# Kernel optimization log

Measured on AMD Instinct MI355X. Metric: run time of the kernel, lower is better.

## Reference

```python
import jax, jax.numpy as jnp
import numpy as np

NUM_HEADS = 16
ROPE_BASE = 10000.0


def _rope_tables(head_dim, seq_len, dtype=jnp.float32):
    # Half-split convention: rotate first half against second half.
    inv_freq = 1.0 / (ROPE_BASE ** (jnp.arange(0, head_dim, 2, dtype=dtype) / head_dim))
    pos = jnp.arange(seq_len, dtype=dtype)
    angles_half = jnp.einsum('s,d->sd', pos, inv_freq)          # (S, D/2)
    angles = jnp.concatenate([angles_half, angles_half], -1)     # (S, D)
    return jnp.cos(angles), jnp.sin(angles)


def _apply_rope(x, cos, sin):
    # x: (H, S, D); cos/sin: (S, D) broadcast over heads
    half = x.shape[-1] // 2
    x1, x2 = x[..., :half], x[..., half:]
    x_rot = jnp.concatenate([-x2, x1], axis=-1)
    return x * cos + x_rot * sin


def setup_inputs() -> dict:
    key = jax.random.key(0)
    S, E = 2048, 2048
    ks = jax.random.split(key, 9)
    sc = 0.02
    return {
        'x': jax.random.normal(ks[0], (S, E), jnp.float32),
        'Wq': jax.random.normal(ks[1], (E, E), jnp.float32) * sc,
        'bq': jax.random.normal(ks[2], (E,), jnp.float32) * sc,
        'Wk': jax.random.normal(ks[3], (E, E), jnp.float32) * sc,
        'bk': jax.random.normal(ks[4], (E,), jnp.float32) * sc,
        'Wv': jax.random.normal(ks[5], (E, E), jnp.float32) * sc,
        'bv': jax.random.normal(ks[6], (E,), jnp.float32) * sc,
        'Wo': jax.random.normal(ks[7], (E, E), jnp.float32) * sc,
        'bo': jax.random.normal(ks[8], (E,), jnp.float32) * sc,
    }


def reference(x, Wq, bq, Wk, bk, Wv, bv, Wo, bo):
    S, E = x.shape
    H = NUM_HEADS
    D = E // H
    scale = D ** 0.5
    cos, sin = _rope_tables(D, S, x.dtype)

    def proj(W, b):
        return (x @ W.T + b).reshape(S, H, D).transpose(1, 0, 2)  # (H, S, D)

    q = _apply_rope(proj(Wq, bq), cos, sin)
    k = _apply_rope(proj(Wk, bk), cos, sin)
    v = proj(Wv, bv)

    scores = jnp.einsum('hsd,htd->hst', q, k) / scale  # (H, S, S)
    attn = jax.nn.softmax(scores, axis=-1)
    out = jnp.einsum('hst,htd->hsd', attn, v)          # (H, S, D)
    # Faithful to the original's transpose(0,1).view(S,E) on a (1,H,S,D)
    # tensor: an in-order (head-major) flatten reinterpreted as (S, E).
    out = out.reshape(S, E)
    return out @ Wo.T + bo
```

## Files before the change

### kernel.cpp

```cpp
#include <hip/hip_runtime.h>

#define SDIM 2048
#define EDIM 2048
#define NHEAD 16
#define DHEAD 128

typedef __attribute__((ext_vector_type(8))) short short8;
typedef __attribute__((ext_vector_type(4))) float floatx4;

__device__ __forceinline__ float bf2f(ushort u) {
    union { uint i; float f; } v; v.i = ((uint)u) << 16; return v.f;
}
__device__ __forceinline__ ushort f2bf(float f) {
    union { float f; uint i; } v; v.f = f;
    uint r = v.i + 0x7fff + ((v.i >> 16) & 1);
    return (ushort)(r >> 16);
}

__device__ __forceinline__ void gload_lds16(const ushort* g, ushort* l) {
    __builtin_amdgcn_global_load_lds(
        (const __attribute__((address_space(1))) void*)g,
        (__attribute__((address_space(3))) void*)l, 16, 0, 0);
}

__global__ void convert5_kernel(
    const float* __restrict__ s0, const float* __restrict__ s1,
    const float* __restrict__ s2, const float* __restrict__ s3,
    const float* __restrict__ s4,
    ushort* __restrict__ d0, ushort* __restrict__ d1,
    ushort* __restrict__ d2, ushort* __restrict__ d3,
    ushort* __restrict__ d4)
{
    const float* src; ushort* dst;
    switch (blockIdx.y) {
        case 0: src = s0; dst = d0; break;
        case 1: src = s1; dst = d1; break;
        case 2: src = s2; dst = d2; break;
        case 3: src = s3; dst = d3; break;
        default: src = s4; dst = d4; break;
    }
    int i = blockIdx.x * blockDim.x + threadIdx.x;
    float4 f = ((const float4*)src)[i];
    ushort4 o;
    o.x = f2bf(f.x); o.y = f2bf(f.y); o.z = f2bf(f.z); o.w = f2bf(f.w);
    ((ushort4*)dst)[i] = o;
}

#define QPRESCALE 0.12754245f

__global__ __launch_bounds__(512, 2) void gemm256_qkv(
    const ushort* __restrict__ A,
    const ushort* __restrict__ B0, const ushort* __restrict__ B1, const ushort* __restrict__ B2,
    const float* __restrict__ s0, const float* __restrict__ s1, const float* __restrict__ s2,
    ushort* __restrict__ C0, ushort* __restrict__ C1, ushort* __restrict__ Vtg)
{
    __shared__ __align__(16) ushort smem[2][2][2][128 * 64];

    const int tid  = threadIdx.x;
    const int lane = tid & 63;
    const int wave = tid >> 6;
    const int l15 = lane & 15, quad = lane >> 4, l7 = lane & 7;
    const int wm = wave & 1, wn = wave >> 1;
    const int bm = blockIdx.x * 256;
    const int which = blockIdx.y >> 3;
    const int n0 = (blockIdx.y & 7) * 256;

    const ushort* Bsel = (which == 0) ? B0 : (which == 1) ? B1 : B2;
    const float*  bia  = (which == 0) ? s0 : (which == 1) ? s1 : s2;

    const int srow = tid >> 3;
    const int sgc  = (((tid & 7) ^ ((tid >> 3) & 7)) << 3);

    floatx4 acc[8][4];
#pragma unroll
    for (int i = 0; i < 8; i++)
#pragma unroll
        for (int j = 0; j < 4; j++) acc[i][j] = (floatx4)0.0f;

    auto stageA = [&](int tile, int h) {
        const ushort* g = A + (size_t)(bm + h * 128 + srow) * EDIM + tile * 64 + sgc;
        ushort* l = &smem[tile & 1][0][h][0] + tid * 8;
        gload_lds16(g, l);
        gload_lds16(g + (size_t)64 * EDIM, l + 4096);
    };
    auto stageB = [&](int tile, int h) {
        const ushort* g = Bsel + (size_t)(n0 + h * 128 + srow) * EDIM + tile * 64 + sgc;
        ushort* l = &smem[tile & 1][1][h][0] + tid * 8;
        gload_lds16(g, l);
        gload_lds16(g + (size_t)64 * EDIM, l + 4096);
    };

    stageA(0, 0); stageA(0, 1); stageB(0, 0); stageB(0, 1);
    stageB(1, 0); stageB(1, 1);
    asm volatile("s_waitcnt vmcnt(4)" ::: "memory");
    __builtin_amdgcn_s_barrier();

    const int c0 = ((quad ^ l7) << 3);
    const int c1 = (((quad + 4) ^ l7) << 3);
    const int brow0 = (wn & 1) * 64;

    short8 af[4][2], bq0[2][2], bq1[2][2];

#define MFMA8(AOFF, NOFF, BQ) \
    _Pragma("unroll") \
    for (int kk = 0; kk < 2; kk++) \
        _Pragma("unroll") \
        for (int mf = 0; mf < 4; mf++) \
            _Pragma("unroll") \
            for (int nf = 0; nf < 2; nf++) \
                acc[(AOFF) + mf][(NOFF) + nf] = __builtin_amdgcn_mfma_f32_16x16x32_bf16( \
                    af[mf][kk], BQ[nf][kk], acc[(AOFF) + mf][(NOFF) + nf], 0, 0, 0);

#define PH_PRE() do { \
    asm volatile("" ::: "memory"); \
    __builtin_amdgcn_s_barrier(); \
    asm volatile("s_waitcnt lgkmcnt(0)" ::: "memory"); \
    __builtin_amdgcn_sched_barrier(0); \
    __builtin_amdgcn_s_setprio(1); \
} while (0)
#define PH_POST() do { \
    __builtin_amdgcn_s_setprio(0); \
    asm volatile("" ::: "memory"); \
    __builtin_amdgcn_s_barrier(); \
} while (0)

    const int NTILES = EDIM / 64;
    for (int t = 0; t < NTILES; ++t) {
        const ushort* aH = &smem[t & 1][0][wm][0];
        const ushort* bH = &smem[t & 1][1][wn >> 1][0];

#pragma unroll
        for (int mf = 0; mf < 4; mf++) {
            const ushort* p = aH + (mf * 16 + l15) * 64;
            af[mf][0] = *(const short8*)(p + c0);
            af[mf][1] = *(const short8*)(p + c1);
        }
#pragma unroll
        for (int nf = 0; nf < 2; nf++) {
            const ushort* p = bH + (brow0 + nf * 16 + l15) * 64;
            bq0[nf][0] = *(const short8*)(p + c0);
            bq0[nf][1] = *(const short8*)(p + c1);
        }
        if (t + 1 < NTILES) stageA(t + 1, 0);
        PH_PRE();
        MFMA8(0, 0, bq0);
        PH_POST();

#pragma unroll
        for (int nf = 0; nf < 2; nf++) {
            const ushort* p = bH + (brow0 + 32 + nf * 16 + l15) * 64;
            bq1[nf][0] = *(const short8*)(p + c0);
            bq1[nf][1] = *(const short8*)(p + c1);
        }
        if (t + 1 < NTILES) stageA(t + 1, 1);
        PH_PRE();
        MFMA8(0, 2, bq1);
        PH_POST();

#pragma unroll
        for (int mf = 0; mf < 4; mf++) {
            const ushort* p = aH + (64 + mf * 16 + l15) * 64;
            af[mf][0] = *(const short8*)(p + c0);
            af[mf][1] = *(const short8*)(p + c1);
        }
        if (t + 2 < NTILES) stageB(t + 2, 0);
        PH_PRE();
        MFMA8(4, 2, bq1);
        PH_POST();

        if (t + 2 < NTILES) stageB(t + 2, 1);
        asm volatile("" ::: "memory");
        __builtin_amdgcn_s_barrier();
        __builtin_amdgcn_s_setprio(1);
        MFMA8(4, 0, bq0);
        __builtin_amdgcn_s_setprio(0);
        if (t < NTILES - 2) asm volatile("s_waitcnt vmcnt(4)" ::: "memory");
        else                asm volatile("s_waitcnt vmcnt(0)" ::: "memory");
        __builtin_amdgcn_s_barrier();
    }
#undef MFMA8
#undef PH_PRE
#undef PH_POST

    if (which == 2) {
#pragma unroll
        for (int an = 0; an < 4; an++) {
            int col = n0 + wn * 64 + an * 16 + l15;
            int h = col >> 7, d = col & 127;
            float bv = bia[col];
            ushort* cp = Vtg + (size_t)h * SDIM * DHEAD + (size_t)d * SDIM;
#pragma unroll
            for (int am = 0; am < 8; am++) {
                int s = bm + wm * 128 + am * 16 + quad * 4;
                ushort4 pk;
                pk.x = f2bf(acc[am][an][0] + bv);
                pk.y = f2bf(acc[am][an][1] + bv);
                pk.z = f2bf(acc[am][an][2] + bv);
                pk.w = f2bf(acc[am][an][3] + bv);
                *(ushort4*)(cp + s) = pk;
            }
        }
    } else {
        ushort* C = (which == 0) ? C0 : C1;
        const float psc = (which == 0) ? QPRESCALE : 1.0f;
        float* xch = (float*)smem;
        float bv[4], invf[4];
#pragma unroll
        for (int an = 0; an < 4; an++) {
            bv[an]   = bia[n0 + wn * 64 + an * 16 + l15];
            invf[an] = __expf((float)(an * 16 + l15) * -0.14391157f);
        }
        const int mybase = wave * 1024 + quad * 16 + l15;
        const int pbase  = (wave ^ 2) * 1024 + quad * 16 + l15;
        const int rowb = bm + wm * 128 + quad * 4;
#pragma unroll
        for (int am = 0; am < 8; am++) {
            __syncthreads();
#pragma unroll
            for (int an = 0; an < 4; an++)
#pragma unroll
                for (int r = 0; r < 4; r++)
                    xch[mybase + an * 256 + r * 64] = acc[am][an][r] + bv[an];
            __syncthreads();
#pragma unroll
            for (int an = 0; an < 4; an++) {
                int col = n0 + wn * 64 + an * 16 + l15;
#pragma unroll
                for (int r = 0; r < 4; r++) {
                    int row = rowb + am * 16 + r;
                    float v = acc[am][an][r] + bv[an];
                    float w = xch[pbase + an * 256 + r * 64];
                    float ang = (float)row * invf[an];
                    float rev = ang * 0.15915494309f;
                    rev -= floorf(rev);
                    float arad = rev * 6.28318530718f;
                    float sn = __sinf(arad), cs = __cosf(arad);
                    float o = ((wn & 1) == 0) ? (v * cs - w * sn) : (v * cs + w * sn);
                    C[(size_t)row * EDIM + col] = f2bf(o * psc);
                }
            }
        }
    }
}

template <typename OUTT, int KSPLIT, int VT_WHICH, bool ROPE>
__global__ __launch_bounds__(256) void gemm_bt(
    const ushort* __restrict__ A,
    const ushort* __restrict__ B0, const ushort* __restrict__ B1, const ushort* __restrict__ B2,
    const float* __restrict__ s0, const float* __restrict__ s1, const float* __restrict__ s2,
    OUTT* __restrict__ C0, OUTT* __restrict__ C1, OUTT* __restrict__ C2,
    int nbpm)
{
    __shared__ __align__(16) ushort smem[2 * 128 * 32];
    ushort* a_s = smem;
    ushort* b_s = smem + 128 * 32;

    const int tid = threadIdx.x;
    const int wave = tid >> 6, lane = tid & 63;
    const int l15 = lane & 15, quad = lane >> 4;
    const int wm = wave & 1, wn = wave >> 1;
    const int bm = blockIdx.x * 128;
    const int which = blockIdx.y / nbpm;
    const int n0 = (blockIdx.y % nbpm) * 128;

    const ushort* B;
    const float*  bia;
    OUTT*         C;
    const ushort* Abase;
    if constexpr (KSPLIT == 2) {
        B = B0; bia = s0; C = C0;
        Abase = A + which * (EDIM / 2);
    } else {
        B   = (which == 0) ? B0 : (which == 1) ? B1 : B2;
        bia = (which == 0) ? s0 : (which == 1) ? s1 : s2;
        C   = (which == 0) ? C0 : (which == 1) ? C1 : C2;
        Abase = A;
    }
    const ushort* Bbase = (KSPLIT == 2) ? B + which * (EDIM / 2) : B;

    floatx4 acc[4][4];
#pragma unroll
    for (int i = 0; i < 4; i++)
#pragma unroll
        for (int j = 0; j < 4; j++) acc[i][j] = (floatx4)0.0f;

    const int t1 = tid + 256;
    const int row0 = tid >> 2, kc0 = (tid & 3) * 8;
    const int row1 = t1 >> 2,  kc1 = (t1 & 3) * 8;

    for (int k0 = 0; k0 < EDIM / KSPLIT; k0 += 32) {
        __syncthreads();
        gload_lds16(Abase + (size_t)(bm + row0) * EDIM + k0 + kc0, a_s + tid * 8);
        gload_lds16(Abase + (size_t)(bm + row1) * EDIM + k0 + kc1, a_s + t1 * 8);
        gload_lds16(Bbase + (size_t)(n0 + row0) * EDIM + k0 + kc0, b_s + tid * 8);
        gload_lds16(Bbase + (size_t)(n0 + row1) * EDIM + k0 + kc1, b_s + t1 * 8);
        __syncthreads();

        short8 af[4], bf[4];
#pragma unroll
        for (int mt = 0; mt < 4; mt++)
            af[mt] = *(const short8*)(a_s + (wm * 64 + mt * 16 + l15) * 32 + quad * 8);
#pragma unroll
        for (int nt = 0; nt < 4; nt++)
            bf[nt] = *(const short8*)(b_s + (wn * 64 + nt * 16 + l15) * 32 + quad * 8);
#pragma unroll
        for (int mt = 0; mt < 4; mt++)
#pragma unroll
            for (int nt = 0; nt < 4; nt++)
                acc[mt][nt] = __builtin_amdgcn_mfma_f32_16x16x32_bf16(af[mt], bf[nt], acc[mt][nt], 0, 0, 0);
    }

    if constexpr (KSPLIT == 2) {
#pragma unroll
        for (int nt = 0; nt < 4; nt++) {
            int col = n0 + wn * 64 + nt * 16 + l15;
            float bv = (which == 0) ? bia[col] : 0.0f;
#pragma unroll
            for (int mt = 0; mt < 4; mt++) {
#pragma unroll
                for (int r = 0; r < 4; r++) {
                    int row = bm + wm * 64 + mt * 16 + quad * 4 + r;
                    atomicAdd(&((float*)C)[(size_t)row * EDIM + col], acc[mt][nt][r] + bv);
                }
            }
        }
    } else {
#pragma unroll
        for (int nt = 0; nt < 4; nt++) {
            int col = n0 + wn * 64 + nt * 16 + l15;
            float bv = bia[col];
#pragma unroll
            for (int mt = 0; mt < 4; mt++) {
#pragma unroll
                for (int r = 0; r < 4; r++) {
                    int row = bm + wm * 64 + mt * 16 + quad * 4 + r;
                    float v = acc[mt][nt][r] + bv;
                    if constexpr (sizeof(OUTT) == 2)
                        ((ushort*)C)[(size_t)row * EDIM + col] = f2bf(v);
                    else
                        ((float*)C)[(size_t)row * EDIM + col] = v;
                }
            }
        }
    }
}

#define MFIX2 17.31234049f
__global__ __launch_bounds__(256, 4) void attn_kernel(
    const ushort* __restrict__ Q, const ushort* __restrict__ K,
    const ushort* __restrict__ Vtg,
    ushort* __restrict__ Opart, float* __restrict__ Lsum,
    ushort* __restrict__ Ab, int nsplit)
{
    __shared__ __align__(16) ushort Ks[64 * 128];
    __shared__ __align__(16) ushort Vt[128 * 64];
    __shared__ __align__(16) ushort Ps[64 * 64];

    const int bid = blockIdx.x;
    const int head = bid & 15, qt = (bid >> 4) & 31, half = bid >> 9;
    const int tid = threadIdx.x, wave = tid >> 6, lane = tid & 63;
    const int l15 = lane & 15, quad = lane >> 4;
    const int l7 = l15 & 7;
    const int kstart = half * (SDIM / nsplit);
    const int ntile = (SDIM / nsplit) / 64;

    short8 qf[4];
    {
        int s = qt * 64 + wave * 16 + l15;
        const ushort* qp = Q + (size_t)s * EDIM + head * DHEAD;
#pragma unroll
        for (int kc = 0; kc < 4; kc++) qf[kc] = *(const short8*)(qp + kc * 32 + quad * 8);
    }

    floatx4 o[8];
#pragma unroll
    for (int i = 0; i < 8; i++) o[i] = (floatx4)0.0f;
    float lsum = 0.0f;

    const int krow = tid >> 4, kc8 = tid & 15;
    const int vd = tid >> 3, vc8 = tid & 7;
    const int prow = wave * 16 + l15;

    for (int kv = 0; kv < ntile; kv++) {
        const int k0 = kstart + kv * 64;
        __syncthreads();
#pragma unroll
        for (int i = 0; i < 4; i++) {
            int row = krow + i * 16;
            uint4 v = *(const uint4*)(K + (size_t)(k0 + row) * EDIM + head * DHEAD + kc8 * 8);
            *(uint4*)(Ks + row * 128 + ((kc8 ^ (row & 7)) << 3)) = v;
        }
#pragma unroll
        for (int i = 0; i < 4; i++) {
            int d = vd + i * 32;
            uint4 v = *(const uint4*)(Vtg + (size_t)head * SDIM * DHEAD + (size_t)d * SDIM + k0 + vc8 * 8);
            *(uint4*)(Vt + d * 64 + ((vc8 ^ (d & 7)) << 3)) = v;
        }
        __syncthreads();

#pragma unroll
        for (int nt = 0; nt < 4; nt++) {
            floatx4 st = (floatx4)0.0f;
#pragma unroll
            for (int kc = 0; kc < 4; kc++) {
                short8 kfr = *(const short8*)(Ks + (nt * 16 + l15) * 128 + (((kc * 4 + quad) ^ l7) << 3));
                st = __builtin_amdgcn_mfma_f32_16x16x32_bf16(kfr, qf[kc], st, 0, 0, 0);
            }
            ushort4 pk;
            float p0 = __builtin_amdgcn_exp2f(st[0] - MFIX2);
            float p1 = __builtin_amdgcn_exp2f(st[1] - MFIX2);
            float p2 = __builtin_amdgcn_exp2f(st[2] - MFIX2);
            float p3 = __builtin_amdgcn_exp2f(st[3] - MFIX2);
            lsum += (p0 + p1) + (p2 + p3);
            pk.x = f2bf(p0); pk.y = f2bf(p1); pk.z = f2bf(p2); pk.w = f2bf(p3);
            int c2 = (nt * 2 + (quad >> 1)) ^ l7;
            *(ushort4*)(Ps + prow * 64 + (c2 << 3) + ((quad & 1) << 2)) = pk;
        }

#pragma unroll
        for (int kc2 = 0; kc2 < 2; kc2++) {
            short8 af = *(const short8*)(Ps + prow * 64 + (((kc2 * 4 + quad) ^ l7) << 3));
#pragma unroll
            for (int nt2 = 0; nt2 < 8; nt2++) {
                short8 bfr = *(const short8*)(Vt + (nt2 * 16 + l15) * 64 + (((kc2 * 4 + quad) ^ l7) << 3));
                o[nt2] = __builtin_amdgcn_mfma_f32_16x16x32_bf16(af, bfr, o[nt2], 0, 0, 0);
            }
        }
    }

    lsum += __shfl_xor(lsum, 16);
    lsum += __shfl_xor(lsum, 32);

    if (nsplit == 1) {
        float invl[4];
#pragma unroll
        for (int r = 0; r < 4; r++) invl[r] = 1.0f / __shfl(lsum, quad * 4 + r, 16);
#pragma unroll
        for (int nt2 = 0; nt2 < 8; nt2++) {
#pragma unroll
            for (int r = 0; r < 4; r++) {
                int s = qt * 64 + wave * 16 + quad * 4 + r;
                int d = nt2 * 16 + l15;
                Ab[(size_t)head * SDIM * DHEAD + (size_t)s * DHEAD + d] = f2bf(o[nt2][r] * invl[r]);
            }
        }
    } else {
        size_t pb = ((size_t)half * NHEAD + head) * SDIM * DHEAD;
#pragma unroll
        for (int nt2 = 0; nt2 < 8; nt2++) {
#pragma unroll
            for (int r = 0; r < 4; r++) {
                int s = qt * 64 + wave * 16 + quad * 4 + r;
                int d = nt2 * 16 + l15;
                Opart[pb + (size_t)s * DHEAD + d] = f2bf(o[nt2][r]);
            }
        }
        if (lane < 16)
            Lsum[((size_t)half * NHEAD + head) * SDIM + qt * 64 + wave * 16 + lane] = lsum;
    }
}

__global__ void merge_kernel(const ushort* __restrict__ Opart,
                             const float* __restrict__ Lsum,
                             ushort* __restrict__ Ab)
{
    const int HS = NHEAD * SDIM;
    int t = blockIdx.x * blockDim.x + threadIdx.x;
    int row = t >> 4, c8 = (t & 15) * 8;
    float inv = 1.0f / (Lsum[row] + Lsum[HS + row] + Lsum[2 * HS + row] + Lsum[3 * HS + row]);
    float acc[8] = {0, 0, 0, 0, 0, 0, 0, 0};
#pragma unroll
    for (int p = 0; p < 4; p++) {
        union { uint4 v; ushort u[8]; } a;
        a.v = *(const uint4*)(Opart + (size_t)p * HS * DHEAD + (size_t)row * DHEAD + c8);
#pragma unroll
        for (int j = 0; j < 8; j++) acc[j] += bf2f(a.u[j]);
    }
    union { uint4 v; ushort u[8]; } ro;
#pragma unroll
    for (int j = 0; j < 8; j++) ro.u[j] = f2bf(acc[j] * inv);
    *(uint4*)(Ab + (size_t)row * DHEAD + c8) = ro.v;
}

extern "C" void kernel_launch(void* const* d_in, const int* in_sizes, int n_in,
                              void* d_out, int out_size, void* d_ws, size_t ws_size,
                              hipStream_t stream) {
    (void)in_sizes; (void)n_in; (void)out_size;
    const float* x  = (const float*)d_in[0];
    const float* Wq = (const float*)d_in[1];
    const float* bq = (const float*)d_in[2];
    const float* Wk = (const float*)d_in[3];
    const float* bk = (const float*)d_in[4];
    const float* Wv = (const float*)d_in[5];
    const float* bv = (const float*)d_in[6];
    const float* Wo = (const float*)d_in[7];
    const float* bo = (const float*)d_in[8];
    float* out = (float*)d_out;

    char* ws = (char*)d_ws;
    const size_t SEG = (size_t)EDIM * EDIM * 2;
    ushort* xb  = (ushort*)(ws + 0 * SEG);
    ushort* Wqb = (ushort*)(ws + 1 * SEG);
    ushort* Wkb = (ushort*)(ws + 2 * SEG);
    ushort* Wvb = (ushort*)(ws + 3 * SEG);
    ushort* Wob = (ushort*)(ws + 4 * SEG);
    ushort* Qb  = (ushort*)(ws + 5 * SEG);
    ushort* Kb  = (ushort*)(ws + 6 * SEG);
    ushort* Vtg = (ushort*)(ws + 7 * SEG);
    ushort* Ab  = (ushort*)(ws + 8 * SEG);
    ushort* Op  = (ushort*)(ws + 0 * SEG);
    float*  Ls  = (float*)(ws + 11 * SEG);

    const int split = (ws_size >= ((size_t)89 << 20)) ? 1 : 0;

    convert5_kernel<<<dim3(4096, 5), 256, 0, stream>>>(
        x, Wq, Wk, Wv, Wo, xb, Wqb, Wkb, Wvb, Wob);

    gemm256_qkv<<<dim3(8, 24), 512, 0, stream>>>(
        xb, Wqb, Wkb, Wvb, bq, bk, bv, Qb, Kb, Vtg);

    if (split) {
        attn_kernel<<<2048, 256, 0, stream>>>(Qb, Kb, Vtg, Op, Ls, Ab, 4);
        merge_kernel<<<2048, 256, 0, stream>>>(Op, Ls, Ab);
        hipMemsetAsync(out, 0, (size_t)EDIM * EDIM * 4, stream);
        gemm_bt<float, 2, -1, false><<<dim3(16, 32), 256, 0, stream>>>(
            Ab, Wob, Wob, Wob, bo, bo, bo, out, out, out, 16);
    } else {
        attn_kernel<<<512, 256, 0, stream>>>(Qb, Kb, Vtg, Op, Ls, Ab, 1);
        gemm_bt<float, 1, -1, false><<<dim3(16, 16), 256, 0, stream>>>(
            Ab, Wob, Wob, Wob, bo, bo, bo, out, out, out, 16);
    }
}
```

Measured before the change: 298.1 us.

## Reuse 256x256 pipelined GEMM for split-K output projection and restructure MFMA k-ordering

Templates the 256-tile QKV GEMM so it also serves the output projection through a split-K mode (two K halves, atomic float adds, bias added only by the first half), replacing the smaller 128-tile gemm_bt in the default split path. The inner loop now loads fragments per k-half instead of per n-half, so each phase runs 16 MFMAs over all four N fragments. It also adds an lgkmcnt wait before the last phase. The RoPE epilogue handles two row-slices per barrier pair, halving the number of syncs. The split-K output path launches only 128 blocks and relies on atomics to a zeroed buffer, which may underfill the GPU and adds atomic traffic.

```diff
diff --git a/kernel.cpp b/kernel.cpp
--- a/kernel.cpp
+++ b/kernel.cpp
@@ -48,11 +48,13 @@
 
 #define QPRESCALE 0.12754245f
 
-__global__ __launch_bounds__(512, 2) void gemm256_qkv(
+template <int MODE>
+__global__ __launch_bounds__(512, 2) void gemm256(
     const ushort* __restrict__ A,
     const ushort* __restrict__ B0, const ushort* __restrict__ B1, const ushort* __restrict__ B2,
     const float* __restrict__ s0, const float* __restrict__ s1, const float* __restrict__ s2,
-    ushort* __restrict__ C0, ushort* __restrict__ C1, ushort* __restrict__ Vtg)
+    ushort* __restrict__ C0, ushort* __restrict__ C1, ushort* __restrict__ Vtg,
+    float* __restrict__ Cf)
 {
     __shared__ __align__(16) ushort smem[2][2][2][128 * 64];
 
@@ -62,11 +64,26 @@
     const int l15 = lane & 15, quad = lane >> 4, l7 = lane & 7;
     const int wm = wave & 1, wn = wave >> 1;
     const int bm = blockIdx.x * 256;
-    const int which = blockIdx.y >> 3;
-    const int n0 = (blockIdx.y & 7) * 256;
-
-    const ushort* Bsel = (which == 0) ? B0 : (which == 1) ? B1 : B2;
-    const float*  bia  = (which == 0) ? s0 : (which == 1) ? s1 : s2;
+
+    int which = 0, ks = 0, n0, NT;
+    const ushort* Abase;
+    const ushort* Bsel;
+    const float*  bia;
+    if constexpr (MODE == 0) {
+        which = blockIdx.y >> 3;
+        n0 = (blockIdx.y & 7) * 256;
+        NT = EDIM / 64;
+        Abase = A;
+        Bsel = (which == 0) ? B0 : (which == 1) ? B1 : B2;
+        bia  = (which == 0) ? s0 : (which == 1) ? s1 : s2;
+    } else {
+        ks = blockIdx.y >> 3;
+        n0 = (blockIdx.y & 7) * 256;
+        NT = (EDIM / 2) / 64;
+        Abase = A + ks * (EDIM / 2);
+        Bsel  = B0 + ks * (EDIM / 2);
+        bia   = s0;
+    }
 
     const int srow = tid >> 3;
     const int sgc  = (((tid & 7) ^ ((tid >> 3) & 7)) << 3);
@@ -78,7 +95,7 @@
         for (int j = 0; j < 4; j++) acc[i][j] = (floatx4)0.0f;
 
     auto stageA = [&](int tile, int h) {
-        const ushort* g = A + (size_t)(bm + h * 128 + srow) * EDIM + tile * 64 + sgc;
+        const ushort* g = Abase + (size_t)(bm + h * 128 + srow) * EDIM + tile * 64 + sgc;
         ushort* l = &smem[tile & 1][0][h][0] + tid * 8;
         gload_lds16(g, l);
         gload_lds16(g + (size_t)64 * EDIM, l + 4096);
@@ -99,17 +116,15 @@
     const int c1 = (((quad + 4) ^ l7) << 3);
     const int brow0 = (wn & 1) * 64;
 
-    short8 af[4][2], bq0[2][2], bq1[2][2];
-
-#define MFMA8(AOFF, NOFF, BQ) \
+    short8 af[4], b0[4], b1[4];
+
+#define MFMA16(AOFF, AF, BF) \
     _Pragma("unroll") \
-    for (int kk = 0; kk < 2; kk++) \
+    for (int mf = 0; mf < 4; mf++) \
         _Pragma("unroll") \
-        for (int mf = 0; mf < 4; mf++) \
-            _Pragma("unroll") \
-            for (int nf = 0; nf < 2; nf++) \
-                acc[(AOFF) + mf][(NOFF) + nf] = __builtin_amdgcn_mfma_f32_16x16x32_bf16( \
-                    af[mf][kk], BQ[nf][kk], acc[(AOFF) + mf][(NOFF) + nf], 0, 0, 0);
+        for (int an = 0; an < 4; an++) \
+            acc[(AOFF) + mf][an] = __builtin_amdgcn_mfma_f32_16x16x32_bf16( \
+                AF[mf], BF[an], acc[(AOFF) + mf][an], 0, 0, 0);
 
 #define PH_PRE() do { \
     asm volatile("" ::: "memory"); \
@@ -124,63 +139,75 @@
     __builtin_amdgcn_s_barrier(); \
 } while (0)
 
-    const int NTILES = EDIM / 64;
-    for (int t = 0; t < NTILES; ++t) {
+    for (int t = 0; t < NT; ++t) {
         const ushort* aH = &smem[t & 1][0][wm][0];
         const ushort* bH = &smem[t & 1][1][wn >> 1][0];
 
 #pragma unroll
-        for (int mf = 0; mf < 4; mf++) {
-            const ushort* p = aH + (mf * 16 + l15) * 64;
-            af[mf][0] = *(const short8*)(p + c0);
-            af[mf][1] = *(const short8*)(p + c1);
-        }
-#pragma unroll
-        for (int nf = 0; nf < 2; nf++) {
-            const ushort* p = bH + (brow0 + nf * 16 + l15) * 64;
-            bq0[nf][0] = *(const short8*)(p + c0);
-            bq0[nf][1] = *(const short8*)(p + c1);
-        }
-        if (t + 1 < NTILES) stageA(t + 1, 0);
+        for (int mf = 0; mf < 4; mf++)
+            af[mf] = *(const short8*)(aH + (mf * 16 + l15) * 64 + c0);
+#pragma unroll
+        for (int an = 0; an < 4; an++)
+            b0[an] = *(const short8*)(bH + (brow0 + an * 16 + l15) * 64 + c0);
+        if (t + 1 < NT) stageA(t + 1, 0);
         PH_PRE();
-        MFMA8(0, 0, bq0);
+        MFMA16(0, af, b0);
         PH_POST();
 
-#pragma unroll
-        for (int nf = 0; nf < 2; nf++) {
-            const ushort* p = bH + (brow0 + 32 + nf * 16 + l15) * 64;
-            bq1[nf][0] = *(const short8*)(p + c0);
-            bq1[nf][1] = *(const short8*)(p + c1);
-        }
-        if (t + 1 < NTILES) stageA(t + 1, 1);
+        short8 ag[4];
+#pragma unroll
+        for (int mf = 0; mf < 4; mf++)
+            ag[mf] = *(const short8*)(aH + (mf * 16 + l15) * 64 + c1);
+#pragma unroll
+        for (int an = 0; an < 4; an++)
+            b1[an] = *(const short8*)(bH + (brow0 + an * 16 + l15) * 64 + c1);
+        if (t + 1 < NT) stageA(t + 1, 1);
         PH_PRE();
-        MFMA8(0, 2, bq1);
+        MFMA16(0, ag, b1);
         PH_POST();
 
 #pragma unroll
-        for (int mf = 0; mf < 4; mf++) {
-            const ushort* p = aH + (64 + mf * 16 + l15) * 64;
-            af[mf][0] = *(const short8*)(p + c0);
-            af[mf][1] = *(const short8*)(p + c1);
-        }
-        if (t + 2 < NTILES) stageB(t + 2, 0);
+        for (int mf = 0; mf < 4; mf++)
+            af[mf] = *(const short8*)(aH + (64 + mf * 16 + l15) * 64 + c0);
+        if (t + 2 < NT) stageB(t + 2, 0);
         PH_PRE();
-        MFMA8(4, 2, bq1);
+        MFMA16(4, af, b0);
         PH_POST();
 
-        if (t + 2 < NTILES) stageB(t + 2, 1);
+#pragma unroll
+        for (int mf = 0; mf < 4; mf++)
+            ag[mf] = *(const short8*)(aH + (64 + mf * 16 + l15) * 64 + c1);
+        if (t + 2 < NT) stageB(t + 2, 1);
         asm volatile("" ::: "memory");
         __builtin_amdgcn_s_barrier();
+        asm volatile("s_waitcnt lgkmcnt(0)" ::: "memory");
+        __builtin_amdgcn_sched_barrier(0);
         __builtin_amdgcn_s_setprio(1);
-        MFMA8(4, 0, bq0);
+        MFMA16(4, ag, b1);
         __builtin_amdgcn_s_setprio(0);
-        if (t < NTILES - 2) asm volatile("s_waitcnt vmcnt(4)" ::: "memory");
-        else                asm volatile("s_waitcnt vmcnt(0)" ::: "memory");
+        if (t < NT - 2) asm volatile("s_waitcnt vmcnt(4)" ::: "memory");
+        else            asm volatile("s_waitcnt vmcnt(0)" ::: "memory");
         __builtin_amdgcn_s_barrier();
     }
-#undef MFMA8
+#undef MFMA16
 #undef PH_PRE
 #undef PH_POST
+
+    if constexpr (MODE == 1) {
+#pragma unroll
+        for (int an = 0; an < 4; an++) {
+            int col = n0 + wn * 64 + an * 16 + l15;
+            float bv = (ks == 0) ? bia[col] : 0.0f;
+#pragma unroll
+            for (int am = 0; am < 8; am++) {
+                int row = bm + wm * 128 + am * 16 + quad * 4;
+#pragma unroll
+                for (int r = 0; r < 4; r++)
+                    atomicAdd(&Cf[(size_t)(row + r) * EDIM + col], acc[am][an][r] + bv);
+            }
+        }
+        return;
+    }
 
     if (which == 2) {
 #pragma unroll
@@ -214,36 +241,44 @@
         const int pbase  = (wave ^ 2) * 1024 + quad * 16 + l15;
         const int rowb = bm + wm * 128 + quad * 4;
 #pragma unroll
-        for (int am = 0; am < 8; am++) {
+        for (int am2 = 0; am2 < 4; am2++) {
             __syncthreads();
 #pragma unroll
-            for (int an = 0; an < 4; an++)
-#pragma unroll
-                for (int r = 0; r < 4; r++)
-                    xch[mybase + an * 256 + r * 64] = acc[am][an][r] + bv[an];
+            for (int sl = 0; sl < 2; sl++) {
+                int am = am2 * 2 + sl;
+#pragma unroll
+                for (int an = 0; an < 4; an++)
+#pragma unroll
+                    for (int r = 0; r < 4; r++)
+                        xch[sl * 8192 + mybase + an * 256 + r * 64] = acc[am][an][r] + bv[an];
+            }
             __syncthreads();
 #pragma unroll
-            for (int an = 0; an < 4; an++) {
-                int col = n0 + wn * 64 + an * 16 + l15;
-#pragma unroll
-                for (int r = 0; r < 4; r++) {
-                    int row = rowb + am * 16 + r;
-                    float v = acc[am][an][r] + bv[an];
-                    float w = xch[pbase + an * 256 + r * 64];
-                    float ang = (float)row * invf[an];
-                    float rev = ang * 0.15915494309f;
-                    rev -= floorf(rev);
-                    float arad = rev * 6.28318530718f;
-                    float sn = __sinf(arad), cs = __cosf(arad);
-                    float o = ((wn & 1) == 0) ? (v * cs - w * sn) : (v * cs + w * sn);
-                    C[(size_t)row * EDIM + col] = f2bf(o * psc);
+            for (int sl = 0; sl < 2; sl++) {
+                int am = am2 * 2 + sl;
+#pragma unroll
+                for (int an = 0; an < 4; an++) {
+                    int col = n0 + wn * 64 + an * 16 + l15;
+#pragma unroll
+                    for (int r = 0; r < 4; r++) {
+                        int row = rowb + am * 16 + r;
+                        float v = acc[am][an][r] + bv[an];
+                        float w = xch[sl * 8192 + pbase + an * 256 + r * 64];
+                        float ang = (float)row * invf[an];
+                        float rev = ang * 0.15915494309f;
+                        rev -= floorf(rev);
+                        float arad = rev * 6.28318530718f;
+                        float sn = __sinf(arad), cs = __cosf(arad);
+                        float o = ((wn & 1) == 0) ? (v * cs - w * sn) : (v * cs + w * sn);
+                        C[(size_t)row * EDIM + col] = f2bf(o * psc);
+                    }
                 }
             }
         }
     }
 }
 
-template <typename OUTT, int KSPLIT, int VT_WHICH, bool ROPE>
+template <typename OUTT, int KSPLIT>
 __global__ __launch_bounds__(256) void gemm_bt(
     const ushort* __restrict__ A,
     const ushort* __restrict__ B0, const ushort* __restrict__ B1, const ushort* __restrict__ B2,
@@ -516,18 +551,19 @@
     convert5_kernel<<<dim3(4096, 5), 256, 0, stream>>>(
         x, Wq, Wk, Wv, Wo, xb, Wqb, Wkb, Wvb, Wob);
 
-    gemm256_qkv<<<dim3(8, 24), 512, 0, stream>>>(
-        xb, Wqb, Wkb, Wvb, bq, bk, bv, Qb, Kb, Vtg);
+    gemm256<0><<<dim3(8, 24), 512, 0, stream>>>(
+        xb, Wqb, Wkb, Wvb, bq, bk, bv, Qb, Kb, Vtg, nullptr);
 
     if (split) {
         attn_kernel<<<2048, 256, 0, stream>>>(Qb, Kb, Vtg, Op, Ls, Ab, 4);
         merge_kernel<<<2048, 256, 0, stream>>>(Op, Ls, Ab);
         hipMemsetAsync(out, 0, (size_t)EDIM * EDIM * 4, stream);
-        gemm_bt<float, 2, -1, false><<<dim3(16, 32), 256, 0, stream>>>(
-            Ab, Wob, Wob, Wob, bo, bo, bo, out, out, out, 16);
+        gemm256<1><<<dim3(8, 16), 512, 0, stream>>>(
+            Ab, Wob, nullptr, nullptr, bo, nullptr, nullptr,
+            nullptr, nullptr, nullptr, out);
     } else {
         attn_kernel<<<512, 256, 0, stream>>>(Qb, Kb, Vtg, Op, Ls, Ab, 1);
-        gemm_bt<float, 1, -1, false><<<dim3(16, 16), 256, 0, stream>>>(
+        gemm_bt<float, 1><<<dim3(16, 16), 256, 0, stream>>>(
             Ab, Wob, Wob, Wob, bo, bo, bo, out, out, out, 16);
     }
 }
```

Result: no change. 299.9 us (+0.6%).
